# Kernel optimization log

Hardware: AMD Instinct MI355X
Metric: run time of the kernel (lower is better)

Reference implementation:

```python
import jax, jax.numpy as jnp
import numpy as np

IN_FEATURES = 4096
OUT_FEATURES = 11008

def setup_inputs() -> dict:
    key = jax.random.key(0)
    k_in, k_w, k_s, k_b = jax.random.split(key, 4)
    inp = jax.random.normal(k_in, (4, 2048, IN_FEATURES), dtype=jnp.float32)
    # int8 quantized weight [out, in]
    weight = jax.random.randint(k_w, (OUT_FEATURES, IN_FEATURES), -127, 128, dtype=jnp.int8)
    # per-output-row scales [out, 1]
    scales = jax.random.uniform(k_s, (OUT_FEATURES, 1), dtype=jnp.float32) * 0.02 + 0.001
    bias = jax.random.normal(k_b, (OUT_FEATURES,), dtype=jnp.float32) * 0.01
    return {"input": inp, "weight": weight, "scales": scales, "bias": bias}

def reference(input, weight, scales, bias):
    # Dequantize: int8 -> core dtype, then per-row scale.  [out, in]
    dequantized_weight = weight.astype(input.dtype) * scales
    # F.linear: input @ W^T + b
    out = jnp.einsum('bsi,oi->bso', input, dequantized_weight) + bias
    return out
```

## Files before the change

### kernel.cpp

```cpp
#include <hip/hip_runtime.h>
#include <stdint.h>

#define M_TOT 8192
#define K_TOT 4096
#define N_TOT 11008
#define BM 256
#define BN 256
#define BK 128
#define NT2 32

typedef __attribute__((ext_vector_type(4))) int i32x4;
typedef __attribute__((ext_vector_type(16))) int i32x16;

__global__ __launch_bounds__(256) void quant_a(const float* __restrict__ a,
                                               int8_t* __restrict__ o,
                                               float* __restrict__ sa) {
  const int row = blockIdx.x;
  const int tid = threadIdx.x;
  const float* ap = a + (size_t)row * K_TOT + tid * 16;
  float4 v[4];
#pragma unroll
  for (int i = 0; i < 4; ++i) v[i] = *(const float4*)(ap + i * 4);
  float m = 0.f;
#pragma unroll
  for (int i = 0; i < 4; ++i) {
    m = fmaxf(m, fmaxf(fmaxf(fabsf(v[i].x), fabsf(v[i].y)),
                       fmaxf(fabsf(v[i].z), fabsf(v[i].w))));
  }
#pragma unroll
  for (int off = 32; off >= 1; off >>= 1)
    m = fmaxf(m, __shfl_xor(m, off));
  __shared__ float red[4];
  if ((tid & 63) == 0) red[tid >> 6] = m;
  __syncthreads();
  float am = fmaxf(fmaxf(red[0], red[1]), fmaxf(red[2], red[3]));
  float inv = am > 0.f ? 127.0f / am : 0.f;
  if (tid == 0) sa[row] = am > 0.f ? am / 127.0f : 0.f;
  union { int8_t b[16]; int4 q; } rr;
#pragma unroll
  for (int i = 0; i < 4; ++i) {
    float4 w = v[i];
    rr.b[i * 4 + 0] = (int8_t)(int)rintf(w.x * inv);
    rr.b[i * 4 + 1] = (int8_t)(int)rintf(w.y * inv);
    rr.b[i * 4 + 2] = (int8_t)(int)rintf(w.z * inv);
    rr.b[i * 4 + 3] = (int8_t)(int)rintf(w.w * inv);
  }
  *(int4*)(o + (size_t)row * K_TOT + tid * 16) = rr.q;
}

__global__ __launch_bounds__(256) void pack_w(const int* __restrict__ w,
                                              int8_t* __restrict__ o, int n16) {
  int stride = gridDim.x * 256;
  for (int i = blockIdx.x * 256 + threadIdx.x; i < n16; i += stride) {
    const int4* p = (const int4*)(w + (size_t)i * 16);
    int4 v0 = p[0], v1 = p[1], v2 = p[2], v3 = p[3];
    int4 r;
    r.x = (v0.x & 0xff) | ((v0.y & 0xff) << 8) | ((v0.z & 0xff) << 16) | (v0.w << 24);
    r.y = (v1.x & 0xff) | ((v1.y & 0xff) << 8) | ((v1.z & 0xff) << 16) | (v1.w << 24);
    r.z = (v2.x & 0xff) | ((v2.y & 0xff) << 8) | ((v2.z & 0xff) << 16) | (v2.w << 24);
    r.w = (v3.x & 0xff) | ((v3.y & 0xff) << 8) | ((v3.z & 0xff) << 16) | (v3.w << 24);
    *(int4*)(o + (size_t)i * 16) = r;
  }
}

#define VM6 asm volatile("s_waitcnt vmcnt(6)" ::: "memory");
#define VM4 asm volatile("s_waitcnt vmcnt(4)" ::: "memory");
#define VM0 asm volatile("s_waitcnt vmcnt(0)" ::: "memory");
#define BAR __builtin_amdgcn_s_barrier();

#define RD_A(BUF, QM, M2, KS) \
  (*(const i32x4*)(lbase + ((BUF)*32768 + (QM)*8192 + (M2)*4096) + va[KS]))
#define RD_B(BUF, NF, KS) \
  (*(const i32x4*)(lbase + ((BUF)*32768 + (NF)*4096) + vb[KS]))

#define STG(OP, Q, BUF, SRC) \
  __builtin_amdgcn_global_load_lds( \
      (const __attribute__((address_space(1))) void*)((SRC) + (size_t)(Q)*64*K_TOT), \
      (__attribute__((address_space(3))) void*)(&lds[OP][BUF][(Q)*8192 + d_off]), 16, 0, 0);

#define BODY(BUF, QM, ...) do {                                                   \
  _Pragma("unroll") for (int m2 = 0; m2 < 2; ++m2)                                \
    _Pragma("unroll") for (int ks = 0; ks < 4; ++ks)                              \
      afr[m2][ks] = RD_A(BUF, QM, m2, ks);                                        \
  if ((QM) == 0) {                                                                \
    _Pragma("unroll") for (int nf = 0; nf < 2; ++nf)                              \
      _Pragma("unroll") for (int ks = 0; ks < 4; ++ks)                            \
        bfr[nf][ks] = RD_B(BUF, nf, ks);                                          \
  }                                                                               \
  __VA_ARGS__                                                                     \
  __builtin_amdgcn_s_setprio(1);                                                  \
  _Pragma("unroll") for (int ks = 0; ks < 4; ++ks)                                \
    _Pragma("unroll") for (int m2 = 0; m2 < 2; ++m2)                              \
      _Pragma("unroll") for (int nf = 0; nf < 2; ++nf)                            \
        acc[(QM)*2 + m2][nf] = __builtin_amdgcn_mfma_i32_32x32x32_i8(             \
            afr[m2][ks], bfr[nf][ks], acc[(QM)*2 + m2][nf], 0, 0, 0);             \
  __builtin_amdgcn_s_setprio(0);                                                  \
} while (0)

__global__ __launch_bounds__(512, 2) void gemm_i8(
    const int8_t* __restrict__ A,
    const int8_t* __restrict__ W,
    const float* __restrict__ sa,
    const float* __restrict__ scales,
    const float* __restrict__ bias,
    float* __restrict__ out) {
  __shared__ __attribute__((aligned(16))) char lds[2][2][32768];

  const int tid = threadIdx.x;
  const int lane = tid & 63;
  const int wid = tid >> 6;
  const int wm = wid >> 2;
  const int wn = wid & 3;
  const int l31 = lane & 31;
  const int hi = lane >> 5;

  const int bid = blockIdx.x;
  const int swz = (bid & 7) * 172 + (bid >> 3);
  const int g = swz / 172;
  const int rem = swz - g * 172;
  const int mq = rem & 3;
  const int mt = g * 4 + mq;
  const int nt = rem >> 2;

  const int r = tid >> 3;
  const int csrc = (tid & 7) ^ (r & 7);
  const int8_t* a_src = A + ((size_t)(mt * 256 + r)) * K_TOT + csrc * 16;
  const int8_t* b_src = W + ((size_t)(nt * 256 + r)) * K_TOT + csrc * 16;
  const int d_off = r * 128 + (tid & 7) * 16;

  int va[4], vb[4];
#pragma unroll
  for (int ks = 0; ks < 4; ++ks) {
    int phys = ((ks * 2 + hi) ^ (l31 & 7)) * 16;
    va[ks] = (wm * 128 + l31) * 128 + phys;
    vb[ks] = 65536 + (wn * 64 + l31) * 128 + phys;
  }
  const char* lbase = (const char*)&lds[0][0][0];

  i32x16 acc[4][2];
#pragma unroll
  for (int i = 0; i < 4; ++i)
#pragma unroll
    for (int j = 0; j < 2; ++j)
#pragma unroll
      for (int e = 0; e < 16; ++e) acc[i][j][e] = 0;
  i32x4 afr[2][4], bfr[2][4];

  STG(0, 0, 0, a_src) STG(0, 2, 0, a_src)
  STG(1, 0, 0, b_src) STG(1, 1, 0, b_src)
  STG(1, 2, 0, b_src) STG(1, 3, 0, b_src)
  STG(0, 1, 0, a_src) STG(0, 3, 0, a_src)
  STG(0, 0, 1, a_src + 128) STG(0, 2, 1, a_src + 128)
  const int8_t* a_nxt = a_src + 128;
  const int8_t* b_nxt = b_src + 128;

  for (int it = 0; it < 15; ++it) {
    VM4 BAR
    BODY(0, 0, STG(1, 0, 1, b_nxt) STG(1, 1, 1, b_nxt)
               STG(1, 2, 1, b_nxt) STG(1, 3, 1, b_nxt));
    VM6 BAR
    BODY(0, 1, STG(0, 1, 1, a_nxt) STG(0, 3, 1, a_nxt)
               STG(0, 0, 0, a_nxt + 128) STG(0, 2, 0, a_nxt + 128));
    a_nxt += 128; b_nxt += 128;
    VM4 BAR
    BODY(1, 0, STG(1, 0, 0, b_nxt) STG(1, 1, 0, b_nxt)
               STG(1, 2, 0, b_nxt) STG(1, 3, 0, b_nxt));
    VM6 BAR
    BODY(1, 1, STG(0, 1, 0, a_nxt) STG(0, 3, 0, a_nxt)
               STG(0, 0, 1, a_nxt + 128) STG(0, 2, 1, a_nxt + 128));
    a_nxt += 128; b_nxt += 128;
  }
  VM4 BAR
  BODY(0, 0, STG(1, 0, 1, b_nxt) STG(1, 1, 1, b_nxt)
             STG(1, 2, 1, b_nxt) STG(1, 3, 1, b_nxt));
  VM6 BAR
  BODY(0, 1, STG(0, 1, 1, a_nxt) STG(0, 3, 1, a_nxt));
  VM0 BAR
  BODY(1, 0, );
  BODY(1, 1, );

  const int ng0 = nt * 256 + wn * 64 + l31;
  const float s0 = scales[ng0], s1 = scales[ng0 + 32];
  const float b0 = bias[ng0], b1 = bias[ng0 + 32];
#pragma unroll
  for (int mf = 0; mf < 4; ++mf) {
    int mb = mt * 256 + wm * 128 + mf * 32 + hi * 4;
#pragma unroll
    for (int reg = 0; reg < 16; ++reg) {
      int m = mb + (reg & 3) + 8 * (reg >> 2);
      float sm = sa[m];
      float* row = out + (size_t)m * N_TOT;
      row[ng0] = (float)acc[mf][0][reg] * (sm * s0) + b0;
      row[ng0 + 32] = (float)acc[mf][1][reg] * (sm * s1) + b1;
    }
  }
}

__global__ __launch_bounds__(256) void naive_gemm(
    const float* __restrict__ a, const int* __restrict__ w,
    const float* __restrict__ scales, const float* __restrict__ bias,
    float* __restrict__ out) {
  size_t total = (size_t)M_TOT * N_TOT;
  size_t stride = (size_t)gridDim.x * 256;
  for (size_t idx = (size_t)blockIdx.x * 256 + threadIdx.x; idx < total; idx += stride) {
    size_t m = idx / N_TOT, n = idx - m * N_TOT;
    const float* ap = a + m * K_TOT;
    const int* wp = w + n * K_TOT;
    float s = 0.f;
    for (int k = 0; k < K_TOT; ++k) s += ap[k] * (float)wp[k];
    out[idx] = s * scales[n] + bias[n];
  }
}

extern "C" void kernel_launch(void* const* d_in, const int* in_sizes, int n_in,
                              void* d_out, int out_size, void* d_ws, size_t ws_size,
                              hipStream_t stream) {
  const float* inp = (const float*)d_in[0];
  const int* w = (const int*)d_in[1];
  const float* sc = (const float*)d_in[2];
  const float* bi = (const float*)d_in[3];
  float* out = (float*)d_out;

  const size_t a_elems = (size_t)M_TOT * K_TOT;
  const size_t w_elems = (size_t)N_TOT * K_TOT;
  const size_t need = 32768 + a_elems + w_elems;

  if (ws_size >= need) {
    float* ws_sa = (float*)d_ws;
    int8_t* ws_a = (int8_t*)d_ws + 32768;
    int8_t* ws_w = ws_a + a_elems;
    quant_a<<<M_TOT, 256, 0, stream>>>(inp, ws_a, ws_sa);
    pack_w<<<2048, 256, 0, stream>>>(w, ws_w, (int)(w_elems / 16));
    gemm_i8<<<(M_TOT / BM) * (N_TOT / BN), 512, 0, stream>>>(ws_a, ws_w, ws_sa, sc, bi, out);
  } else {
    naive_gemm<<<4096, 256, 0, stream>>>(inp, w, sc, bi, out);
  }
}
```

Before: 491.4 us.

## Switch int8 GEMM to 16x16x64 MFMA with merged full-K-tile windows

Replaces the 32x32x32 int8 MFMA with the 16x16x64 variant and processes a whole 128-wide K tile per barrier window instead of two half-windows. Fragment loads, swizzled LDS offsets, the accumulator layout and the epilogue are rewritten to match. The waitcnt/barrier schedule drops to one barrier per buffer, and the two-blocks-per-CU launch bound is removed. This is meant to cut barrier count and raise MFMA throughput, at the cost of more live fragment registers, which may lower occupancy.

```diff
diff --git a/kernel.cpp b/kernel.cpp
--- a/kernel.cpp
+++ b/kernel.cpp
@@ -7,10 +7,8 @@
 #define BM 256
 #define BN 256
 #define BK 128
-#define NT2 32
 
 typedef __attribute__((ext_vector_type(4))) int i32x4;
-typedef __attribute__((ext_vector_type(16))) int i32x16;
 
 __global__ __launch_bounds__(256) void quant_a(const float* __restrict__ a,
                                                int8_t* __restrict__ o,
@@ -63,56 +61,70 @@
   }
 }
 
-#define VM6 asm volatile("s_waitcnt vmcnt(6)" ::: "memory");
-#define VM4 asm volatile("s_waitcnt vmcnt(4)" ::: "memory");
+#define VM2 asm volatile("s_waitcnt vmcnt(2)" ::: "memory");
 #define VM0 asm volatile("s_waitcnt vmcnt(0)" ::: "memory");
 #define BAR __builtin_amdgcn_s_barrier();
-
-#define RD_A(BUF, QM, M2, KS) \
-  (*(const i32x4*)(lbase + ((BUF)*32768 + (QM)*8192 + (M2)*4096) + va[KS]))
-#define RD_B(BUF, NF, KS) \
-  (*(const i32x4*)(lbase + ((BUF)*32768 + (NF)*4096) + vb[KS]))
+#define SCHED0 __builtin_amdgcn_sched_barrier(0);
+
+#define RD_A(BUF, QM, MF, KS) \
+  (*(const i32x4*)(lbase + ((BUF)*32768 + (QM)*8192 + (MF)*2048) + aoff[KS]))
+#define RD_B(BUF, J, KS) \
+  (*(const i32x4*)(lbase + (65536 + (BUF)*32768 + (J)*2048) + boff[KS]))
 
 #define STG(OP, Q, BUF, SRC) \
   __builtin_amdgcn_global_load_lds( \
       (const __attribute__((address_space(1))) void*)((SRC) + (size_t)(Q)*64*K_TOT), \
-      (__attribute__((address_space(3))) void*)(&lds[OP][BUF][(Q)*8192 + d_off]), 16, 0, 0);
-
-#define BODY(BUF, QM, ...) do {                                                   \
-  _Pragma("unroll") for (int m2 = 0; m2 < 2; ++m2)                                \
-    _Pragma("unroll") for (int ks = 0; ks < 4; ++ks)                              \
-      afr[m2][ks] = RD_A(BUF, QM, m2, ks);                                        \
-  if ((QM) == 0) {                                                                \
-    _Pragma("unroll") for (int nf = 0; nf < 2; ++nf)                              \
-      _Pragma("unroll") for (int ks = 0; ks < 4; ++ks)                            \
-        bfr[nf][ks] = RD_B(BUF, nf, ks);                                          \
+      (__attribute__((address_space(3))) void*)(lds + (OP)*65536 + (BUF)*32768 + (Q)*8192 + d_off), 16, 0, 0);
+
+#define WINDOW(BUF, VMW, STGB, STGA13, STGA02) do {                               \
+  VMW                                                                             \
+  BAR                                                                             \
+  _Pragma("unroll") for (int mf = 0; mf < 4; ++mf) {                              \
+    a0[mf][0] = RD_A(BUF, 0, mf, 0);                                              \
+    a0[mf][1] = RD_A(BUF, 0, mf, 1);                                              \
   }                                                                               \
-  __VA_ARGS__                                                                     \
+  _Pragma("unroll") for (int j = 0; j < 4; ++j) {                                 \
+    bb[j][0] = RD_B(BUF, j, 0);                                                   \
+    bb[j][1] = RD_B(BUF, j, 1);                                                   \
+  }                                                                               \
+  _Pragma("unroll") for (int mf = 0; mf < 4; ++mf) {                              \
+    a1[mf][0] = RD_A(BUF, 1, mf, 0);                                              \
+    a1[mf][1] = RD_A(BUF, 1, mf, 1);                                              \
+  }                                                                               \
+  STGB                                                                            \
+  STGA13                                                                          \
   __builtin_amdgcn_s_setprio(1);                                                  \
-  _Pragma("unroll") for (int ks = 0; ks < 4; ++ks)                                \
-    _Pragma("unroll") for (int m2 = 0; m2 < 2; ++m2)                              \
-      _Pragma("unroll") for (int nf = 0; nf < 2; ++nf)                            \
-        acc[(QM)*2 + m2][nf] = __builtin_amdgcn_mfma_i32_32x32x32_i8(             \
-            afr[m2][ks], bfr[nf][ks], acc[(QM)*2 + m2][nf], 0, 0, 0);             \
+  _Pragma("unroll") for (int ks = 0; ks < 2; ++ks)                                \
+    _Pragma("unroll") for (int mf = 0; mf < 4; ++mf)                              \
+      _Pragma("unroll") for (int j = 0; j < 4; ++j)                               \
+        acc[mf][j] = __builtin_amdgcn_mfma_i32_16x16x64_i8(                       \
+            a0[mf][ks], bb[j][ks], acc[mf][j], 0, 0, 0);                          \
+  _Pragma("unroll") for (int ks = 0; ks < 2; ++ks)                                \
+    _Pragma("unroll") for (int mf = 0; mf < 4; ++mf)                              \
+      _Pragma("unroll") for (int j = 0; j < 4; ++j)                               \
+        acc[4 + mf][j] = __builtin_amdgcn_mfma_i32_16x16x64_i8(                   \
+            a1[mf][ks], bb[j][ks], acc[4 + mf][j], 0, 0, 0);                      \
   __builtin_amdgcn_s_setprio(0);                                                  \
+  SCHED0                                                                          \
+  STGA02                                                                          \
 } while (0)
 
-__global__ __launch_bounds__(512, 2) void gemm_i8(
+__global__ __launch_bounds__(512) void gemm_i8(
     const int8_t* __restrict__ A,
     const int8_t* __restrict__ W,
     const float* __restrict__ sa,
     const float* __restrict__ scales,
     const float* __restrict__ bias,
     float* __restrict__ out) {
-  __shared__ __attribute__((aligned(16))) char lds[2][2][32768];
+  __shared__ __attribute__((aligned(16))) char lds[131072];
 
   const int tid = threadIdx.x;
   const int lane = tid & 63;
   const int wid = tid >> 6;
   const int wm = wid >> 2;
   const int wn = wid & 3;
-  const int l31 = lane & 31;
-  const int hi = lane >> 5;
+  const int l15 = lane & 15;
+  const int l4 = lane >> 4;
 
   const int bid = blockIdx.x;
   const int swz = (bid & 7) * 172 + (bid >> 3);
@@ -128,70 +140,64 @@
   const int8_t* b_src = W + ((size_t)(nt * 256 + r)) * K_TOT + csrc * 16;
   const int d_off = r * 128 + (tid & 7) * 16;
 
-  int va[4], vb[4];
-#pragma unroll
-  for (int ks = 0; ks < 4; ++ks) {
-    int phys = ((ks * 2 + hi) ^ (l31 & 7)) * 16;
-    va[ks] = (wm * 128 + l31) * 128 + phys;
-    vb[ks] = 65536 + (wn * 64 + l31) * 128 + phys;
-  }
-  const char* lbase = (const char*)&lds[0][0][0];
-
-  i32x16 acc[4][2];
-#pragma unroll
-  for (int i = 0; i < 4; ++i)
-#pragma unroll
-    for (int j = 0; j < 2; ++j)
-#pragma unroll
-      for (int e = 0; e < 16; ++e) acc[i][j][e] = 0;
-  i32x4 afr[2][4], bfr[2][4];
+  const int xm = l15 & 7;
+  const int pc0 = l4 ^ xm;
+  const int pc1 = pc0 ^ 4;
+  int aoff[2], boff[2];
+  aoff[0] = (wm * 128 + l15) * 128 + pc0 * 16;
+  aoff[1] = (wm * 128 + l15) * 128 + pc1 * 16;
+  boff[0] = (wn * 64 + l15) * 128 + pc0 * 16;
+  boff[1] = (wn * 64 + l15) * 128 + pc1 * 16;
+  const char* lbase = lds;
+
+  i32x4 acc[8][4];
+#pragma unroll
+  for (int i = 0; i < 8; ++i)
+#pragma unroll
+    for (int j = 0; j < 4; ++j) {
+      i32x4 z = {0, 0, 0, 0};
+      acc[i][j] = z;
+    }
+  i32x4 a0[4][2], a1[4][2], bb[4][2];
 
   STG(0, 0, 0, a_src) STG(0, 2, 0, a_src)
-  STG(1, 0, 0, b_src) STG(1, 1, 0, b_src)
-  STG(1, 2, 0, b_src) STG(1, 3, 0, b_src)
+  STG(1, 0, 0, b_src) STG(1, 1, 0, b_src) STG(1, 2, 0, b_src) STG(1, 3, 0, b_src)
   STG(0, 1, 0, a_src) STG(0, 3, 0, a_src)
   STG(0, 0, 1, a_src + 128) STG(0, 2, 1, a_src + 128)
   const int8_t* a_nxt = a_src + 128;
   const int8_t* b_nxt = b_src + 128;
 
   for (int it = 0; it < 15; ++it) {
-    VM4 BAR
-    BODY(0, 0, STG(1, 0, 1, b_nxt) STG(1, 1, 1, b_nxt)
-               STG(1, 2, 1, b_nxt) STG(1, 3, 1, b_nxt));
-    VM6 BAR
-    BODY(0, 1, STG(0, 1, 1, a_nxt) STG(0, 3, 1, a_nxt)
-               STG(0, 0, 0, a_nxt + 128) STG(0, 2, 0, a_nxt + 128));
+    WINDOW(0, VM2,
+        STG(1, 0, 1, b_nxt) STG(1, 1, 1, b_nxt) STG(1, 2, 1, b_nxt) STG(1, 3, 1, b_nxt),
+        STG(0, 1, 1, a_nxt) STG(0, 3, 1, a_nxt),
+        STG(0, 0, 0, a_nxt + 128) STG(0, 2, 0, a_nxt + 128));
     a_nxt += 128; b_nxt += 128;
-    VM4 BAR
-    BODY(1, 0, STG(1, 0, 0, b_nxt) STG(1, 1, 0, b_nxt)
-               STG(1, 2, 0, b_nxt) STG(1, 3, 0, b_nxt));
-    VM6 BAR
-    BODY(1, 1, STG(0, 1, 0, a_nxt) STG(0, 3, 0, a_nxt)
-               STG(0, 0, 1, a_nxt + 128) STG(0, 2, 1, a_nxt + 128));
+    WINDOW(1, VM2,
+        STG(1, 0, 0, b_nxt) STG(1, 1, 0, b_nxt) STG(1, 2, 0, b_nxt) STG(1, 3, 0, b_nxt),
+        STG(0, 1, 0, a_nxt) STG(0, 3, 0, a_nxt),
+        STG(0, 0, 1, a_nxt + 128) STG(0, 2, 1, a_nxt + 128));
     a_nxt += 128; b_nxt += 128;
   }
-  VM4 BAR
-  BODY(0, 0, STG(1, 0, 1, b_nxt) STG(1, 1, 1, b_nxt)
-             STG(1, 2, 1, b_nxt) STG(1, 3, 1, b_nxt));
-  VM6 BAR
-  BODY(0, 1, STG(0, 1, 1, a_nxt) STG(0, 3, 1, a_nxt));
-  VM0 BAR
-  BODY(1, 0, );
-  BODY(1, 1, );
-
-  const int ng0 = nt * 256 + wn * 64 + l31;
-  const float s0 = scales[ng0], s1 = scales[ng0 + 32];
-  const float b0 = bias[ng0], b1 = bias[ng0 + 32];
-#pragma unroll
-  for (int mf = 0; mf < 4; ++mf) {
-    int mb = mt * 256 + wm * 128 + mf * 32 + hi * 4;
-#pragma unroll
-    for (int reg = 0; reg < 16; ++reg) {
-      int m = mb + (reg & 3) + 8 * (reg >> 2);
-      float sm = sa[m];
-      float* row = out + (size_t)m * N_TOT;
-      row[ng0] = (float)acc[mf][0][reg] * (sm * s0) + b0;
-      row[ng0 + 32] = (float)acc[mf][1][reg] * (sm * s1) + b1;
+  WINDOW(0, VM2,
+      STG(1, 0, 1, b_nxt) STG(1, 1, 1, b_nxt) STG(1, 2, 1, b_nxt) STG(1, 3, 1, b_nxt),
+      STG(0, 1, 1, a_nxt) STG(0, 3, 1, a_nxt),
+      );
+  WINDOW(1, VM0, , , );
+
+#pragma unroll
+  for (int j = 0; j < 4; ++j) {
+    int n_g = nt * 256 + wn * 64 + j * 16 + l15;
+    float s = scales[n_g];
+    float b = bias[n_g];
+#pragma unroll
+    for (int i = 0; i < 8; ++i) {
+      int m0 = mt * 256 + wm * 128 + i * 16 + l4 * 4;
+#pragma unroll
+      for (int jj = 0; jj < 4; ++jj) {
+        int m = m0 + jj;
+        out[(size_t)m * N_TOT + n_g] = (float)acc[i][j][jj] * (sa[m] * s) + b;
+      }
     }
   }
 }
```

After: 488.4 us. About the same (-0.6%).
